# Performance work log

Measured on AMD Instinct MI355X. Metric: run time of the kernel, lower is better.

Reference implementation:

```python
import jax, jax.numpy as jnp
import numpy as np

ALPHA = 0.2  # LeakyReLU negative slope
NEG_INF = -9e15


def setup_inputs() -> dict:
    key = jax.random.key(0)
    ks = jax.random.split(key, 6)
    B, N, F_IN, F_OUT = 4, 1024, 64, 64
    h = jax.random.normal(ks[0], (B, N, F_IN), dtype=jnp.float32)
    adj = jax.random.randint(ks[1], (B, N, N), 0, 2, dtype=jnp.int32)
    lin_w = jax.random.normal(ks[2], (F_OUT, F_IN), dtype=jnp.float32) * (1.0 / np.sqrt(F_IN))
    lin_b = jax.random.normal(ks[3], (F_OUT,), dtype=jnp.float32) * 0.02
    W_w = jax.random.normal(ks[4], (F_OUT, 2 * F_OUT), dtype=jnp.float32) * (1.0 / np.sqrt(2 * F_OUT))
    a = jax.random.normal(ks[5], (F_OUT, 1), dtype=jnp.float32) * (1.414 / np.sqrt(F_OUT))
    return {"h": h, "adj": adj, "lin_w": lin_w, "lin_b": lin_b, "W_w": W_w, "a": a}


def reference(h, adj, lin_w, lin_b, W_w, a):
    F_OUT = lin_w.shape[0]
    # h' = Linear(h): (B, N, F_OUT)
    hp = jnp.einsum('bni,oi->bno', h, lin_w) + lin_b
    # W @ concat(h_i, h_j) == h_i @ W1^T + h_j @ W2^T  (same math, no 2F concat)
    W1, W2 = W_w[:, :F_OUT], W_w[:, F_OUT:]
    u = jnp.einsum('bnf,of->bno', hp, W1)  # source/row term   (B, N, F_OUT)
    v = jnp.einsum('bnf,of->bno', hp, W2)  # target/col term   (B, N, F_OUT)
    s = u[:, :, None, :] + v[:, None, :, :]        # (B, N, N, F_OUT)
    s = jnp.where(s > 0, s, ALPHA * s)             # LeakyReLU
    e = jnp.einsum('bijf,f->bij', s, a[:, 0])      # (B, N, N)
    e = jnp.where(adj > 0, e, NEG_INF)
    attention = jax.nn.softmax(e, axis=2)
    h_prime = jnp.einsum('bij,bjf->bif', attention, hp)
    return jax.nn.elu(h_prime)
```

## Files before the change

### kernel.cpp

```cpp
#include <hip/hip_runtime.h>
#include <hip/hip_bf16.h>
#include <math.h>

constexpr int B = 4;
constexpr int N = 1024;
constexpr int F = 64;
constexpr float NEGINF = -9000000000000000.0f;

__global__ __launch_bounds__(256) void gat_prep(
    const float* __restrict__ h, const float* __restrict__ lin_w,
    const float* __restrict__ lin_b, const float* __restrict__ W_w,
    float* __restrict__ hp, float* __restrict__ ug, float* __restrict__ vT) {
  __shared__ float hT[64 * 68];
  __shared__ float wT[64 * 68];
  __shared__ float w1T[64 * 68];
  __shared__ float w2T[64 * 68];
  __shared__ float hpT[64 * 68];
  const int b = blockIdx.x >> 4;
  const int n0 = (blockIdx.x & 15) << 6;
  const int tid = threadIdx.x;

  for (int idx = tid; idx < 4096; idx += 256) {
    const int r = idx >> 6, c = idx & 63;
    hT[c * 68 + r] = h[((b << 10) + n0 + r) * 64 + c];
    wT[c * 68 + r] = lin_w[idx];
    w1T[c * 68 + r] = W_w[r * 128 + c];
    w2T[c * 68 + r] = W_w[r * 128 + 64 + c];
  }
  __syncthreads();

  const int tf = tid & 15, tn = tid >> 4;
  float acc[4][4];
#pragma unroll
  for (int q = 0; q < 4; ++q)
#pragma unroll
    for (int r = 0; r < 4; ++r) acc[q][r] = lin_b[tf * 4 + r];

#pragma unroll 4
  for (int k = 0; k < 64; ++k) {
    const float4 ha = *(const float4*)&hT[k * 68 + tn * 4];
    const float4 wa = *(const float4*)&wT[k * 68 + tf * 4];
    const float hv[4] = {ha.x, ha.y, ha.z, ha.w};
    const float wv[4] = {wa.x, wa.y, wa.z, wa.w};
#pragma unroll
    for (int q = 0; q < 4; ++q)
#pragma unroll
      for (int r = 0; r < 4; ++r) acc[q][r] = fmaf(hv[q], wv[r], acc[q][r]);
  }
#pragma unroll
  for (int q = 0; q < 4; ++q) {
    const float4 o4 = make_float4(acc[q][0], acc[q][1], acc[q][2], acc[q][3]);
    *(float4*)&hp[((b << 10) + n0 + tn * 4 + q) * 64 + tf * 4] = o4;
#pragma unroll
    for (int r = 0; r < 4; ++r) hpT[(tf * 4 + r) * 68 + tn * 4 + q] = acc[q][r];
  }
  __syncthreads();

  float au[4][4], av[4][4];
#pragma unroll
  for (int q = 0; q < 4; ++q)
#pragma unroll
    for (int r = 0; r < 4; ++r) { au[q][r] = 0.f; av[q][r] = 0.f; }

#pragma unroll 4
  for (int k = 0; k < 64; ++k) {
    const float4 ha = *(const float4*)&hpT[k * 68 + tn * 4];
    const float4 w1 = *(const float4*)&w1T[k * 68 + tf * 4];
    const float4 w2 = *(const float4*)&w2T[k * 68 + tf * 4];
    const float hv[4] = {ha.x, ha.y, ha.z, ha.w};
    const float v1[4] = {w1.x, w1.y, w1.z, w1.w};
    const float v2[4] = {w2.x, w2.y, w2.z, w2.w};
#pragma unroll
    for (int q = 0; q < 4; ++q)
#pragma unroll
      for (int r = 0; r < 4; ++r) {
        au[q][r] = fmaf(hv[q], v1[r], au[q][r]);
        av[q][r] = fmaf(hv[q], v2[r], av[q][r]);
      }
  }
#pragma unroll
  for (int q = 0; q < 4; ++q) {
    const float4 o4 = make_float4(au[q][0], au[q][1], au[q][2], au[q][3]);
    *(float4*)&ug[((b << 10) + n0 + tn * 4 + q) * 64 + tf * 4] = o4;
  }
#pragma unroll
  for (int q = 0; q < 4; ++q)
#pragma unroll
    for (int r = 0; r < 4; ++r) hT[(tf * 4 + r) * 68 + tn * 4 + q] = av[q][r];
  __syncthreads();
  for (int idx = tid; idx < 4096; idx += 256) {
    const int o = idx >> 6, n = idx & 63;
    vT[((b << 6) + o) * N + n0 + n] = hT[o * 68 + n];
  }
}

__global__ __launch_bounds__(256) void gat_attn(
    const float* __restrict__ ug, const float* __restrict__ vT,
    const float* __restrict__ hp, const int* __restrict__ adj,
    const float* __restrict__ a, float* __restrict__ out) {
  __shared__ float e_s[N * 12];
  __shared__ float u_s[64 * 8];
  __shared__ float a_s[64];
  __shared__ float red_s[4 * 8 * 64];
  __shared__ float rinv_s[8];

  const int b = blockIdx.x >> 7;
  const int i0 = (blockIdx.x & 127) << 3;
  const int tid = threadIdx.x;

  if (tid < 64) a_s[tid] = a[tid];
  for (int idx = tid; idx < 512; idx += 256)
    u_s[(idx & 63) * 8 + (idx >> 6)] =
        ug[((b << 10) + i0 + (idx >> 6)) * 64 + (idx & 63)];
  __syncthreads();

  float e[8][4];
#pragma unroll
  for (int i = 0; i < 8; ++i)
#pragma unroll
    for (int k = 0; k < 4; ++k) e[i][k] = 0.f;

  const float* vb = vT + (b << 6) * N;
#pragma unroll 2
  for (int f = 0; f < 64; ++f) {
    const float ap = a_s[f];
    float vv[4];
#pragma unroll
    for (int k = 0; k < 4; ++k) vv[k] = vb[(f << 10) + tid + (k << 8)];
    const float4 ua = *(const float4*)&u_s[f * 8];
    const float4 ub = *(const float4*)&u_s[f * 8 + 4];
    const float uu[8] = {ua.x, ua.y, ua.z, ua.w, ub.x, ub.y, ub.z, ub.w};
#pragma unroll
    for (int i = 0; i < 8; ++i)
#pragma unroll
      for (int k = 0; k < 4; ++k) {
        const float t = uu[i] + vv[k];
        e[i][k] = fmaf(ap, fmaxf(t, 0.2f * t), e[i][k]);
      }
  }
  const int* adjb = adj + ((b << 10) + i0) * N;
#pragma unroll
  for (int i = 0; i < 8; ++i)
#pragma unroll
    for (int k = 0; k < 4; ++k) {
      const int ad = adjb[i * N + tid + (k << 8)];
      e_s[(tid + (k << 8)) * 12 + i] = ad > 0 ? e[i][k] : NEGINF;
    }
  __syncthreads();

  const int lane = tid & 63, w = tid >> 6;
#pragma unroll
  for (int ii = 0; ii < 2; ++ii) {
    const int i = (w << 1) + ii;
    float m = -INFINITY;
#pragma unroll
    for (int mm = 0; mm < 16; ++mm) m = fmaxf(m, e_s[(lane + (mm << 6)) * 12 + i]);
#pragma unroll
    for (int off = 32; off; off >>= 1) m = fmaxf(m, __shfl_xor(m, off));
    float s = 0.f;
#pragma unroll
    for (int mm = 0; mm < 16; ++mm) {
      const int idx = (lane + (mm << 6)) * 12 + i;
      const float p = __expf(e_s[idx] - m);
      e_s[idx] = p;
      s += p;
    }
#pragma unroll
    for (int off = 32; off; off >>= 1) s += __shfl_xor(s, off);
    if (lane == 0) rinv_s[i] = 1.0f / s;
  }
  __syncthreads();

  const int fl = tid & 63, g = tid >> 6;
  float acc[8];
#pragma unroll
  for (int i = 0; i < 8; ++i) acc[i] = 0.f;
  const float* hpb = hp + ((b << 10) << 6);
#pragma unroll 4
  for (int jj = g << 8; jj < (g << 8) + 256; ++jj) {
    const float hv = hpb[(jj << 6) + fl];
    const float4 p0 = *(const float4*)&e_s[jj * 12];
    const float4 p1 = *(const float4*)&e_s[jj * 12 + 4];
    acc[0] = fmaf(p0.x, hv, acc[0]);
    acc[1] = fmaf(p0.y, hv, acc[1]);
    acc[2] = fmaf(p0.z, hv, acc[2]);
    acc[3] = fmaf(p0.w, hv, acc[3]);
    acc[4] = fmaf(p1.x, hv, acc[4]);
    acc[5] = fmaf(p1.y, hv, acc[5]);
    acc[6] = fmaf(p1.z, hv, acc[6]);
    acc[7] = fmaf(p1.w, hv, acc[7]);
  }
#pragma unroll
  for (int i = 0; i < 8; ++i) red_s[((g << 3) + i) * 64 + fl] = acc[i];
  __syncthreads();

#pragma unroll
  for (int o = 0; o < 2; ++o) {
    const int idx = tid + (o << 8);
    const int i = idx >> 6, f = idx & 63;
    float v = red_s[i * 64 + f] + red_s[(8 + i) * 64 + f] +
              red_s[(16 + i) * 64 + f] + red_s[(24 + i) * 64 + f];
    v *= rinv_s[i];
    out[((b << 10) + i0 + i) * 64 + f] = v > 0.f ? v : expm1f(v);
  }
}

extern "C" void kernel_launch(void* const* d_in, const int* in_sizes, int n_in,
                              void* d_out, int out_size, void* d_ws, size_t ws_size,
                              hipStream_t stream) {
  const float* h = (const float*)d_in[0];
  const int* adj = (const int*)d_in[1];
  const float* lin_w = (const float*)d_in[2];
  const float* lin_b = (const float*)d_in[3];
  const float* W_w = (const float*)d_in[4];
  const float* a = (const float*)d_in[5];
  float* outp = (float*)d_out;

  float* hp = (float*)d_ws;
  float* ug = hp + B * N * F;
  float* vT = ug + B * N * F;

  gat_prep<<<dim3(64), dim3(256), 0, stream>>>(h, lin_w, lin_b, W_w, hp, ug, vT);
  gat_attn<<<dim3(512), dim3(256), 0, stream>>>(ug, vT, hp, adj, a, outp);
}
```

Before: 134.8 us.

## Rewrite LeakyReLU via abs identity, fold weights, keep softmax in registers

```diff
diff --git a/kernel.cpp b/kernel.cpp
--- a/kernel.cpp
+++ b/kernel.cpp
@@ -4,114 +4,175 @@
 
 constexpr int B = 4;
 constexpr int N = 1024;
-constexpr int F = 64;
 constexpr float NEGINF = -9000000000000000.0f;
+
+__global__ __launch_bounds__(512) void gat_wk0(
+    const float* __restrict__ lin_w, const float* __restrict__ lin_b,
+    const float* __restrict__ W_w, float* __restrict__ Wu, float* __restrict__ Wv,
+    float* __restrict__ bu, float* __restrict__ bv) {
+  __shared__ float lw[64 * 68];
+  __shared__ float ww[64 * 132];
+  __shared__ float lb[64];
+  const int tid = threadIdx.x;
+  for (int idx = tid; idx < 4096; idx += 512)
+    lw[(idx >> 6) * 68 + (idx & 63)] = lin_w[idx];
+  for (int idx = tid; idx < 8192; idx += 512)
+    ww[(idx >> 7) * 132 + (idx & 127)] = W_w[idx];
+  if (tid < 64) lb[tid] = lin_b[tid];
+  __syncthreads();
+
+  const int f = tid >> 3, i0 = (tid & 7) << 3;
+  float wua[8], wva[8];
+#pragma unroll
+  for (int r = 0; r < 8; ++r) { wua[r] = 0.f; wva[r] = 0.f; }
+  float bup = 0.f, bvp = 0.f;
+#pragma unroll 4
+  for (int o = 0; o < 64; ++o) {
+    const float w1 = ww[f * 132 + o];
+    const float w2 = ww[f * 132 + 64 + o];
+    const float4 A = *(const float4*)&lw[o * 68 + i0];
+    const float4 Bv = *(const float4*)&lw[o * 68 + i0 + 4];
+    const float lv[8] = {A.x, A.y, A.z, A.w, Bv.x, Bv.y, Bv.z, Bv.w};
+#pragma unroll
+    for (int r = 0; r < 8; ++r) {
+      wua[r] = fmaf(w1, lv[r], wua[r]);
+      wva[r] = fmaf(w2, lv[r], wva[r]);
+    }
+    bup = fmaf(w1, lb[o], bup);
+    bvp = fmaf(w2, lb[o], bvp);
+  }
+  *(float4*)&Wu[f * 64 + i0] = make_float4(wua[0], wua[1], wua[2], wua[3]);
+  *(float4*)&Wu[f * 64 + i0 + 4] = make_float4(wua[4], wua[5], wua[6], wua[7]);
+  *(float4*)&Wv[f * 64 + i0] = make_float4(wva[0], wva[1], wva[2], wva[3]);
+  *(float4*)&Wv[f * 64 + i0 + 4] = make_float4(wva[4], wva[5], wva[6], wva[7]);
+  if ((tid & 7) == 0) { bu[f] = bup; bv[f] = bvp; }
+}
 
 __global__ __launch_bounds__(256) void gat_prep(
     const float* __restrict__ h, const float* __restrict__ lin_w,
-    const float* __restrict__ lin_b, const float* __restrict__ W_w,
-    float* __restrict__ hp, float* __restrict__ ug, float* __restrict__ vT) {
-  __shared__ float hT[64 * 68];
-  __shared__ float wT[64 * 68];
-  __shared__ float w1T[64 * 68];
-  __shared__ float w2T[64 * 68];
-  __shared__ float hpT[64 * 68];
-  const int b = blockIdx.x >> 4;
-  const int n0 = (blockIdx.x & 15) << 6;
+    const float* __restrict__ lin_b, const float* __restrict__ a_g,
+    const float* __restrict__ Wu, const float* __restrict__ Wv,
+    const float* __restrict__ bu_g, const float* __restrict__ bv_g,
+    float* __restrict__ hp, float* __restrict__ u_out, float* __restrict__ vT,
+    float* __restrict__ au_out, float* __restrict__ av_out) {
+  __shared__ float hs[64 * 34];
+  __shared__ float wl[64 * 68];
+  __shared__ float wu[64 * 68];
+  __shared__ float wv[64 * 68];
+  __shared__ float vt_s[64 * 33];
+  __shared__ float ared[2][32 * 17];
+  __shared__ float lb_s[64], bu_s[64], bv_s[64], a_s[64];
+
+  const int b = blockIdx.x >> 5;
+  const int n0 = (blockIdx.x & 31) << 5;
   const int tid = threadIdx.x;
 
+  for (int idx = tid; idx < 2048; idx += 256) {
+    const int r = idx >> 6, c = idx & 63;
+    hs[c * 34 + r] = h[((b << 10) + n0 + r) * 64 + c];
+  }
   for (int idx = tid; idx < 4096; idx += 256) {
     const int r = idx >> 6, c = idx & 63;
-    hT[c * 68 + r] = h[((b << 10) + n0 + r) * 64 + c];
-    wT[c * 68 + r] = lin_w[idx];
-    w1T[c * 68 + r] = W_w[r * 128 + c];
-    w2T[c * 68 + r] = W_w[r * 128 + 64 + c];
+    wl[c * 68 + r] = lin_w[idx];
+    wu[c * 68 + r] = Wu[idx];
+    wv[c * 68 + r] = Wv[idx];
+  }
+  if (tid < 64) {
+    lb_s[tid] = lin_b[tid]; bu_s[tid] = bu_g[tid];
+    bv_s[tid] = bv_g[tid];  a_s[tid] = a_g[tid];
   }
   __syncthreads();
 
   const int tf = tid & 15, tn = tid >> 4;
-  float acc[4][4];
-#pragma unroll
-  for (int q = 0; q < 4; ++q)
-#pragma unroll
-    for (int r = 0; r < 4; ++r) acc[q][r] = lin_b[tf * 4 + r];
-
+  float ahp[2][4], aU[2][4], aV[2][4];
+#pragma unroll
+  for (int q = 0; q < 2; ++q)
+#pragma unroll
+    for (int r = 0; r < 4; ++r) {
+      ahp[q][r] = lb_s[tf * 4 + r];
+      aU[q][r] = bu_s[tf * 4 + r];
+      aV[q][r] = bv_s[tf * 4 + r];
+    }
 #pragma unroll 4
   for (int k = 0; k < 64; ++k) {
-    const float4 ha = *(const float4*)&hT[k * 68 + tn * 4];
-    const float4 wa = *(const float4*)&wT[k * 68 + tf * 4];
-    const float hv[4] = {ha.x, ha.y, ha.z, ha.w};
-    const float wv[4] = {wa.x, wa.y, wa.z, wa.w};
-#pragma unroll
-    for (int q = 0; q < 4; ++q)
-#pragma unroll
-      for (int r = 0; r < 4; ++r) acc[q][r] = fmaf(hv[q], wv[r], acc[q][r]);
-  }
-#pragma unroll
-  for (int q = 0; q < 4; ++q) {
-    const float4 o4 = make_float4(acc[q][0], acc[q][1], acc[q][2], acc[q][3]);
-    *(float4*)&hp[((b << 10) + n0 + tn * 4 + q) * 64 + tf * 4] = o4;
-#pragma unroll
-    for (int r = 0; r < 4; ++r) hpT[(tf * 4 + r) * 68 + tn * 4 + q] = acc[q][r];
-  }
-  __syncthreads();
-
-  float au[4][4], av[4][4];
-#pragma unroll
-  for (int q = 0; q < 4; ++q)
-#pragma unroll
-    for (int r = 0; r < 4; ++r) { au[q][r] = 0.f; av[q][r] = 0.f; }
-
-#pragma unroll 4
-  for (int k = 0; k < 64; ++k) {
-    const float4 ha = *(const float4*)&hpT[k * 68 + tn * 4];
-    const float4 w1 = *(const float4*)&w1T[k * 68 + tf * 4];
-    const float4 w2 = *(const float4*)&w2T[k * 68 + tf * 4];
-    const float hv[4] = {ha.x, ha.y, ha.z, ha.w};
-    const float v1[4] = {w1.x, w1.y, w1.z, w1.w};
-    const float v2[4] = {w2.x, w2.y, w2.z, w2.w};
-#pragma unroll
-    for (int q = 0; q < 4; ++q)
+    const float2 h2 = *(const float2*)&hs[k * 34 + tn * 2];
+    const float hv[2] = {h2.x, h2.y};
+    const float4 l4 = *(const float4*)&wl[k * 68 + tf * 4];
+    const float4 u4 = *(const float4*)&wu[k * 68 + tf * 4];
+    const float4 v4 = *(const float4*)&wv[k * 68 + tf * 4];
+    const float lv[4] = {l4.x, l4.y, l4.z, l4.w};
+    const float uv[4] = {u4.x, u4.y, u4.z, u4.w};
+    const float vv[4] = {v4.x, v4.y, v4.z, v4.w};
+#pragma unroll
+    for (int q = 0; q < 2; ++q)
 #pragma unroll
       for (int r = 0; r < 4; ++r) {
-        au[q][r] = fmaf(hv[q], v1[r], au[q][r]);
-        av[q][r] = fmaf(hv[q], v2[r], av[q][r]);
+        ahp[q][r] = fmaf(hv[q], lv[r], ahp[q][r]);
+        aU[q][r] = fmaf(hv[q], uv[r], aU[q][r]);
+        aV[q][r] = fmaf(hv[q], vv[r], aV[q][r]);
       }
   }
 #pragma unroll
-  for (int q = 0; q < 4; ++q) {
-    const float4 o4 = make_float4(au[q][0], au[q][1], au[q][2], au[q][3]);
-    *(float4*)&ug[((b << 10) + n0 + tn * 4 + q) * 64 + tf * 4] = o4;
-  }
-#pragma unroll
-  for (int q = 0; q < 4; ++q)
-#pragma unroll
-    for (int r = 0; r < 4; ++r) hT[(tf * 4 + r) * 68 + tn * 4 + q] = av[q][r];
-  __syncthreads();
-  for (int idx = tid; idx < 4096; idx += 256) {
-    const int o = idx >> 6, n = idx & 63;
-    vT[((b << 6) + o) * N + n0 + n] = hT[o * 68 + n];
+  for (int q = 0; q < 2; ++q) {
+    const int row = (b << 10) + n0 + tn * 2 + q;
+    *(float4*)&hp[row * 64 + tf * 4] =
+        make_float4(ahp[q][0], ahp[q][1], ahp[q][2], ahp[q][3]);
+    *(float4*)&u_out[row * 64 + tf * 4] =
+        make_float4(aU[q][0], aU[q][1], aU[q][2], aU[q][3]);
+  }
+  float aup[2] = {0.f, 0.f}, avp[2] = {0.f, 0.f};
+#pragma unroll
+  for (int q = 0; q < 2; ++q)
+#pragma unroll
+    for (int r = 0; r < 4; ++r) {
+      vt_s[(tf * 4 + r) * 33 + tn * 2 + q] = aV[q][r];
+      aup[q] = fmaf(a_s[tf * 4 + r], aU[q][r], aup[q]);
+      avp[q] = fmaf(a_s[tf * 4 + r], aV[q][r], avp[q]);
+    }
+#pragma unroll
+  for (int q = 0; q < 2; ++q) {
+    ared[0][(tn * 2 + q) * 17 + tf] = aup[q];
+    ared[1][(tn * 2 + q) * 17 + tf] = avp[q];
+  }
+  __syncthreads();
+  for (int idx = tid; idx < 2048; idx += 256) {
+    const int f = idx >> 5, n = idx & 31;
+    vT[(((b << 6) + f) << 10) + n0 + n] = vt_s[f * 33 + n];
+  }
+  if (tid < 64) {
+    const int which = tid >> 5, row = tid & 31;
+    float s2 = 0.f;
+#pragma unroll
+    for (int t = 0; t < 16; ++t) s2 += ared[which][row * 17 + t];
+    if (which == 0) au_out[(b << 10) + n0 + row] = s2;
+    else av_out[(b << 10) + n0 + row] = s2;
   }
 }
 
 __global__ __launch_bounds__(256) void gat_attn(
-    const float* __restrict__ ug, const float* __restrict__ vT,
+    const float* __restrict__ u_g, const float* __restrict__ vT,
     const float* __restrict__ hp, const int* __restrict__ adj,
-    const float* __restrict__ a, float* __restrict__ out) {
-  __shared__ float e_s[N * 12];
+    const float* __restrict__ a_g, const float* __restrict__ au_g,
+    const float* __restrict__ av_g, float* __restrict__ out) {
+  __shared__ float p_s[2 * 1024 * 4];
   __shared__ float u_s[64 * 8];
   __shared__ float a_s[64];
-  __shared__ float red_s[4 * 8 * 64];
+  __shared__ float au_s[8];
+  __shared__ float wred[4 * 8];
+  __shared__ float wsum[4 * 8];
   __shared__ float rinv_s[8];
 
   const int b = blockIdx.x >> 7;
   const int i0 = (blockIdx.x & 127) << 3;
   const int tid = threadIdx.x;
-
-  if (tid < 64) a_s[tid] = a[tid];
-  for (int idx = tid; idx < 512; idx += 256)
-    u_s[(idx & 63) * 8 + (idx >> 6)] =
-        ug[((b << 10) + i0 + (idx >> 6)) * 64 + (idx & 63)];
+  const int lane = tid & 63, w = tid >> 6;
+
+  if (tid < 64) a_s[tid] = a_g[tid];
+  if (tid < 8) au_s[tid] = au_g[(b << 10) + i0 + tid];
+  for (int idx = tid; idx < 512; idx += 256) {
+    const int i = idx >> 6, f = idx & 63;
+    u_s[f * 8 + i] = u_g[((b << 10) + i0 + i) * 64 + f];
+  }
   __syncthreads();
 
   float e[8][4];
@@ -120,10 +181,10 @@
 #pragma unroll
     for (int k = 0; k < 4; ++k) e[i][k] = 0.f;
 
-  const float* vb = vT + (b << 6) * N;
+  const float* vb = vT + ((b << 6) << 10);
 #pragma unroll 2
   for (int f = 0; f < 64; ++f) {
-    const float ap = a_s[f];
+    const float af = a_s[f];
     float vv[4];
 #pragma unroll
     for (int k = 0; k < 4; ++k) vv[k] = vb[(f << 10) + tid + (k << 8)];
@@ -133,41 +194,56 @@
 #pragma unroll
     for (int i = 0; i < 8; ++i)
 #pragma unroll
-      for (int k = 0; k < 4; ++k) {
-        const float t = uu[i] + vv[k];
-        e[i][k] = fmaf(ap, fmaxf(t, 0.2f * t), e[i][k]);
-      }
-  }
-  const int* adjb = adj + ((b << 10) + i0) * N;
+      for (int k = 0; k < 4; ++k)
+        e[i][k] = fmaf(af, fabsf(uu[i] + vv[k]), e[i][k]);
+  }
+  float avv[4];
+#pragma unroll
+  for (int k = 0; k < 4; ++k)
+    avv[k] = 0.6f * av_g[(b << 10) + tid + (k << 8)];
+  float au6[8];
+#pragma unroll
+  for (int i = 0; i < 8; ++i) au6[i] = 0.6f * au_s[i];
+  const int* adjb = adj + ((((b << 10) + i0)) << 10) + tid;
 #pragma unroll
   for (int i = 0; i < 8; ++i)
 #pragma unroll
     for (int k = 0; k < 4; ++k) {
-      const int ad = adjb[i * N + tid + (k << 8)];
-      e_s[(tid + (k << 8)) * 12 + i] = ad > 0 ? e[i][k] : NEGINF;
+      const float ev = fmaf(0.4f, e[i][k], au6[i] + avv[k]);
+      e[i][k] = adjb[(i << 10) + (k << 8)] > 0 ? ev : NEGINF;
     }
-  __syncthreads();
-
-  const int lane = tid & 63, w = tid >> 6;
-#pragma unroll
-  for (int ii = 0; ii < 2; ++ii) {
-    const int i = (w << 1) + ii;
-    float m = -INFINITY;
-#pragma unroll
-    for (int mm = 0; mm < 16; ++mm) m = fmaxf(m, e_s[(lane + (mm << 6)) * 12 + i]);
-#pragma unroll
-    for (int off = 32; off; off >>= 1) m = fmaxf(m, __shfl_xor(m, off));
-    float s = 0.f;
-#pragma unroll
-    for (int mm = 0; mm < 16; ++mm) {
-      const int idx = (lane + (mm << 6)) * 12 + i;
-      const float p = __expf(e_s[idx] - m);
-      e_s[idx] = p;
-      s += p;
-    }
-#pragma unroll
-    for (int off = 32; off; off >>= 1) s += __shfl_xor(s, off);
-    if (lane == 0) rinv_s[i] = 1.0f / s;
+
+#pragma unroll
+  for (int i = 0; i < 8; ++i) {
+    float mm = fmaxf(fmaxf(e[i][0], e[i][1]), fmaxf(e[i][2], e[i][3]));
+#pragma unroll
+    for (int off = 32; off; off >>= 1) mm = fmaxf(mm, __shfl_xor(mm, off));
+    if (lane == 0) wred[w * 8 + i] = mm;
+  }
+  __syncthreads();
+#pragma unroll
+  for (int i = 0; i < 8; ++i) {
+    const float mi = fmaxf(fmaxf(wred[i], wred[8 + i]),
+                           fmaxf(wred[16 + i], wred[24 + i]));
+#pragma unroll
+    for (int k = 0; k < 4; ++k) e[i][k] = __expf(e[i][k] - mi);
+    float ss = e[i][0] + e[i][1] + e[i][2] + e[i][3];
+#pragma unroll
+    for (int off = 32; off; off >>= 1) ss += __shfl_xor(ss, off);
+    if (lane == 0) wsum[w * 8 + i] = ss;
+  }
+  __syncthreads();
+#pragma unroll
+  for (int i = 0; i < 8; ++i) {
+    const float stot = wsum[i] + wsum[8 + i] + wsum[16 + i] + wsum[24 + i];
+    if (tid == i) rinv_s[i] = 1.0f / stot;
+  }
+#pragma unroll
+  for (int k = 0; k < 4; ++k) {
+    const int j = tid + (k << 8);
+    *(float4*)&p_s[j << 2] = make_float4(e[0][k], e[1][k], e[2][k], e[3][k]);
+    *(float4*)&p_s[4096 + (j << 2)] =
+        make_float4(e[4][k], e[5][k], e[6][k], e[7][k]);
   }
   __syncthreads();
 
@@ -175,12 +251,12 @@
   float acc[8];
 #pragma unroll
   for (int i = 0; i < 8; ++i) acc[i] = 0.f;
-  const float* hpb = hp + ((b << 10) << 6);
+  const float* hpb = hp + (b << 16);
 #pragma unroll 4
   for (int jj = g << 8; jj < (g << 8) + 256; ++jj) {
     const float hv = hpb[(jj << 6) + fl];
-    const float4 p0 = *(const float4*)&e_s[jj * 12];
-    const float4 p1 = *(const float4*)&e_s[jj * 12 + 4];
+    const float4 p0 = *(const float4*)&p_s[jj << 2];
+    const float4 p1 = *(const float4*)&p_s[4096 + (jj << 2)];
     acc[0] = fmaf(p0.x, hv, acc[0]);
     acc[1] = fmaf(p0.y, hv, acc[1]);
     acc[2] = fmaf(p0.z, hv, acc[2]);
@@ -190,18 +266,19 @@
     acc[6] = fmaf(p1.z, hv, acc[6]);
     acc[7] = fmaf(p1.w, hv, acc[7]);
   }
-#pragma unroll
-  for (int i = 0; i < 8; ++i) red_s[((g << 3) + i) * 64 + fl] = acc[i];
-  __syncthreads();
-
+  __syncthreads();
+  float* red = p_s;
+#pragma unroll
+  for (int i = 0; i < 8; ++i) red[((g << 3) + i) << 6 | fl] = acc[i];
+  __syncthreads();
 #pragma unroll
   for (int o = 0; o < 2; ++o) {
     const int idx = tid + (o << 8);
     const int i = idx >> 6, f = idx & 63;
-    float v = red_s[i * 64 + f] + red_s[(8 + i) * 64 + f] +
-              red_s[(16 + i) * 64 + f] + red_s[(24 + i) * 64 + f];
-    v *= rinv_s[i];
-    out[((b << 10) + i0 + i) * 64 + f] = v > 0.f ? v : expm1f(v);
+    float r = red[(i << 6) + f] + red[((8 + i) << 6) + f] +
+              red[((16 + i) << 6) + f] + red[((24 + i) << 6) + f];
+    r *= rinv_s[i];
+    out[((b << 10) + i0 + i) * 64 + f] = r > 0.f ? r : expm1f(r);
   }
 }
 
@@ -216,10 +293,19 @@
   const float* a = (const float*)d_in[5];
   float* outp = (float*)d_out;
 
-  float* hp = (float*)d_ws;
-  float* ug = hp + B * N * F;
-  float* vT = ug + B * N * F;
-
-  gat_prep<<<dim3(64), dim3(256), 0, stream>>>(h, lin_w, lin_b, W_w, hp, ug, vT);
-  gat_attn<<<dim3(512), dim3(256), 0, stream>>>(ug, vT, hp, adj, a, outp);
+  float* ws = (float*)d_ws;
+  float* hp = ws;
+  float* u = ws + 262144;
+  float* vT = ws + 524288;
+  float* au = ws + 786432;
+  float* av = ws + 790528;
+  float* Wu = ws + 794624;
+  float* Wv = ws + 798720;
+  float* bu = ws + 802816;
+  float* bv = ws + 802880;
+
+  gat_wk0<<<dim3(1), dim3(512), 0, stream>>>(lin_w, lin_b, W_w, Wu, Wv, bu, bv);
+  gat_prep<<<dim3(128), dim3(256), 0, stream>>>(h, lin_w, lin_b, a, Wu, Wv, bu,
+                                                bv, hp, u, vT, au, av);
+  gat_attn<<<dim3(512), dim3(256), 0, stream>>>(u, vT, hp, adj, a, au, av, outp);
 }
```

Result: no change. 135.6 us (+0.6%).
